# Performance work log

Hardware: AMD Instinct MI355X
Metric: run time of the kernel (lower is better)

## Reference

```python
import jax, jax.numpy as jnp
import numpy as np

EMB = 1024
N_HEAD = 16
HEAD = 64
D_FF = 4 * EMB
LN_EPS = 1e-5


def layernorm(x, g, b):
    mu = jnp.mean(x, axis=-1, keepdims=True)
    var = jnp.mean(jnp.square(x - mu), axis=-1, keepdims=True)
    return (x - mu) * jax.lax.rsqrt(var + LN_EPS) * g + b


def setup_inputs() -> dict:
    key = jax.random.key(0)
    ks = jax.random.split(key, 12)
    s = 0.02
    x = jax.random.normal(ks[0], (4, 2048, EMB), dtype=jnp.float32)
    # per-head Q/K/V projections (no bias), stacked along head axis
    Wq = jax.random.normal(ks[1], (N_HEAD, EMB, HEAD), dtype=jnp.float32) * s
    Wk = jax.random.normal(ks[2], (N_HEAD, EMB, HEAD), dtype=jnp.float32) * s
    Wv = jax.random.normal(ks[3], (N_HEAD, EMB, HEAD), dtype=jnp.float32) * s
    Wo = jax.random.normal(ks[4], (EMB, EMB), dtype=jnp.float32) * s
    bo = jnp.zeros((EMB,), dtype=jnp.float32)
    ln1_g = jnp.ones((EMB,), dtype=jnp.float32)
    ln1_b = jnp.zeros((EMB,), dtype=jnp.float32)
    W1 = jax.random.normal(ks[5], (EMB, D_FF), dtype=jnp.float32) * s
    b1 = jnp.zeros((D_FF,), dtype=jnp.float32)
    W2 = jax.random.normal(ks[6], (D_FF, EMB), dtype=jnp.float32) * s
    b2 = jnp.zeros((EMB,), dtype=jnp.float32)
    ln2_g = jnp.ones((EMB,), dtype=jnp.float32)
    ln2_b = jnp.zeros((EMB,), dtype=jnp.float32)
    return dict(x=x, Wq=Wq, Wk=Wk, Wv=Wv, Wo=Wo, bo=bo, ln1_g=ln1_g,
                ln1_b=ln1_b, W1=W1, b1=b1, W2=W2, b2=b2, ln2_g=ln2_g,
                ln2_b=ln2_b)


def reference(x, Wq, Wk, Wv, Wo, bo, ln1_g, ln1_b, W1, b1, W2, b2, ln2_g, ln2_b):
    B, T, _ = x.shape
    # fused multi-head QKV (equivalent to the per-head Python loop + concat)
    q = jnp.einsum('btd,hdk->bhtk', x, Wq)
    k = jnp.einsum('btd,hdk->bhtk', x, Wk)
    v = jnp.einsum('btd,hdk->bhtk', x, Wv)
    scores = jnp.einsum('bhtk,bhsk->bhts', q, k) / jnp.sqrt(jnp.float32(HEAD))
    att = jax.nn.softmax(scores, axis=-1)
    heads = jnp.einsum('bhts,bhsk->bhtk', att, v)           # [B,H,T,head]
    cat = heads.transpose(0, 2, 1, 3).reshape(B, T, EMB)     # concat over heads
    mha = cat @ Wo + bo
    x = x + layernorm(mha, ln1_g, ln1_b)                     # residual of LN(sublayer)
    ff = jax.nn.gelu(x @ W1 + b1, approximate=False) @ W2 + b2
    x = x + layernorm(ff, ln2_g, ln2_b)
    return x
```

## Files before the change

kernel.cpp:

```cpp
#include <hip/hip_runtime.h>
#include <math.h>


using u16 = unsigned short;
typedef __bf16 bf16x8 __attribute__((ext_vector_type(8)));
typedef __bf16 bf16x4 __attribute__((ext_vector_type(4)));
typedef unsigned short u16x8 __attribute__((ext_vector_type(8)));
typedef unsigned short u16x4 __attribute__((ext_vector_type(4)));
typedef float f32x4 __attribute__((ext_vector_type(4)));

#if defined(__has_builtin)
#if __has_builtin(__builtin_amdgcn_exp2f)
#define EXP2F(x) __builtin_amdgcn_exp2f(x)
#endif
#endif
#ifndef EXP2F
#define EXP2F(x) __expf((x) * 0.69314718055994531f)
#endif

__device__ __forceinline__ float bf2f(u16 h) {
  return __uint_as_float(((unsigned int)h) << 16);
}
__device__ __forceinline__ u16 f2bf(float f) {
  unsigned int u = __float_as_uint(f);
  u += 0x7fffu + ((u >> 16) & 1u);
  return (u16)(u >> 16);
}

__device__ __forceinline__ void gload_lds16(const void* g, void* l) {
  __builtin_amdgcn_global_load_lds(
      (__attribute__((address_space(1))) void*)(g),
      (__attribute__((address_space(3))) void*)(l), 16, 0, 0);
}

__global__ __launch_bounds__(256) void detect_dtype(const u16* __restrict__ x,
                                                    int* __restrict__ flag) {
  __shared__ int cnt[256];
  int c = 0;
#pragma unroll
  for (int j = 0; j < 8; ++j) {
    float v = bf2f(x[threadIdx.x * 8 + j]);
    float a = fabsf(v);
    if (a >= 1e-4f && a <= 64.0f) ++c;
  }
  cnt[threadIdx.x] = c;
  __syncthreads();
  if (threadIdx.x == 0) {
    int t = 0;
    for (int i = 0; i < 256; ++i) t += cnt[i];
    flag[0] = (t < 1638) ? 1 : 0;
  }
}

__global__ __launch_bounds__(256) void cvt_copy(const void* __restrict__ in,
                                                u16* __restrict__ out,
                                                const int* __restrict__ flagp,
                                                long n) {
  long idx = ((long)blockIdx.x * 256 + threadIdx.x) * 4;
  if (idx >= n) return;
  if (*flagp) {
    float4 v = *(const float4*)((const float*)in + idx);
    out[idx] = f2bf(v.x); out[idx + 1] = f2bf(v.y);
    out[idx + 2] = f2bf(v.z); out[idx + 3] = f2bf(v.w);
  } else {
    *(u16x4*)(out + idx) = *(const u16x4*)((const u16*)in + idx);
  }
}

__global__ __launch_bounds__(256) void cvt_vecs(
    const void* s0, const void* s1, const void* s2, const void* s3,
    const void* s4, const void* s5, const void* s6, u16* __restrict__ dst,
    const int* __restrict__ flagp) {
  const int lens[7] = {1024, 1024, 1024, 4096, 1024, 1024, 1024};
  const int offs[7] = {0, 1024, 2048, 3072, 7168, 8192, 9216};
  const void* srcs[7] = {s0, s1, s2, s3, s4, s5, s6};
  int w = blockIdx.x;
  int f = *flagp;
  for (int i = threadIdx.x; i < lens[w]; i += 256)
    dst[offs[w] + i] = f ? f2bf(((const float*)srcs[w])[i])
                         : ((const u16*)srcs[w])[i];
}

__global__ __launch_bounds__(256) void transpose_cvt(
    const void* __restrict__ in, u16* __restrict__ out, int R, int C,
    long inBS, long outBS, const int* __restrict__ flagp) {
  __shared__ u16 tile[32][33];
  int f = *flagp;
  u16* ob = out + (long)blockIdx.z * outBS;
  int c = blockIdx.x * 32 + threadIdx.x;
  int r0 = blockIdx.y * 32;
  if (f) {
    const float* ib = (const float*)in + (long)blockIdx.z * inBS;
#pragma unroll
    for (int i = threadIdx.y; i < 32; i += 8)
      tile[i][threadIdx.x] = f2bf(ib[(long)(r0 + i) * C + c]);
  } else {
    const u16* ib = (const u16*)in + (long)blockIdx.z * inBS;
#pragma unroll
    for (int i = threadIdx.y; i < 32; i += 8)
      tile[i][threadIdx.x] = ib[(long)(r0 + i) * C + c];
  }
  __syncthreads();
  int r = r0 + threadIdx.x;
  int c0 = blockIdx.x * 32;
#pragma unroll
  for (int i = threadIdx.y; i < 32; i += 8)
    ob[(long)(c0 + i) * R + r] = tile[threadIdx.x][i];
}

__global__ __launch_bounds__(256) void kv_frag(const u16* __restrict__ qkv,
                                               u16* __restrict__ KF,
                                               u16* __restrict__ VF) {
  __shared__ u16 Kt[64][72];
  __shared__ u16 Vt[64][72];
  const int jblk = blockIdx.x, bh = blockIdx.y;
  const int b = bh >> 4, h = bh & 15;
  const int tid = threadIdx.x;
  const long j0 = jblk * 64;

  {
    int tt = tid >> 2, c0 = (tid & 3) * 16;
    const u16* src = qkv + (long)(b * 2048 + j0 + tt) * 3072 + h * 64 + c0;
    *(u16x8*)(&Kt[tt][c0]) = *(const u16x8*)(src + 1024);
    *(u16x8*)(&Kt[tt][c0 + 8]) = *(const u16x8*)(src + 1024 + 8);
    *(u16x8*)(&Vt[tt][c0]) = *(const u16x8*)(src + 2048);
    *(u16x8*)(&Vt[tt][c0 + 8]) = *(const u16x8*)(src + 2048 + 8);
  }
  __syncthreads();

  long obase = ((long)bh * 32 + jblk) * 8 * 512;
#pragma unroll
  for (int si = 0; si < 2; ++si) {
    int s = tid * 2 + si;
    int f = s >> 6, ln = s & 63;
    int kt = f >> 2, nt = f & 3;
    int lr = ln & 15, lq = ln >> 4;
    u16x8 ko, vo;
#pragma unroll
    for (int j = 0; j < 8; ++j) {
      ko[j] = Kt[nt * 16 + lr][kt * 32 + lq * 8 + j];
      vo[j] = Vt[kt * 32 + lq * 8 + j][nt * 16 + lr];
    }
    *(u16x8*)(KF + obase + (long)s * 8) = ko;
    *(u16x8*)(VF + obase + (long)s * 8) = vo;
  }
}

__device__ __forceinline__ bf16x8 fragld(const u16* lb, int row, int ks,
                                         int lq) {
  int slot = ((ks << 2) | lq) ^ (row & 7);
  return *(const bf16x8*)(lb + row * 64 + slot * 8);
}

template <int EPI, int BN>
__global__ __launch_bounds__(512, 2) void gemm2ph(
    const u16* __restrict__ A, const u16* __restrict__ Bt,
    const u16* __restrict__ bias, u16* __restrict__ Cout,
    int M, int N, int K) {
  static_assert(BN == 256 || BN == 128, "");
  constexpr int NFQ = BN / 128;
  __shared__ u16 As[2][16384];
  __shared__ u16 Bs[2][BN * 64];
  const int tid = threadIdx.x;
  const int wave = tid >> 6, lane = tid & 63;
  const int lr = lane & 15, lq = lane >> 4;

  const int MT = M >> 8, NTt = N / BN;
  const int nwg = MT * NTt;
  int wg = blockIdx.x;
  if (!(nwg & 7)) wg = (wg & 7) * (nwg >> 3) + (wg >> 3);
  const int tm = wg % MT, tn = wg / MT;
  const long m0 = (long)tm << 8;
  const long n0 = (long)tn * BN;

  const int wm = (wave >> 2) << 7;
  const int wn = (wave & 3) * (BN / 4);

  const int srow = lane >> 3;
  const int skoff = ((lane & 7) ^ srow) * 8;

  auto stage = [&](int buf, int t) {
#pragma unroll
    for (int j = 0; j < 4; ++j)
      gload_lds16(
          A + (m0 + j * 64 + wave * 8 + srow) * (long)K + t * 64 + skoff,
          &As[buf][j * 4096 + (wave << 9)]);
#pragma unroll
    for (int j = 0; j < BN / 64; ++j)
      gload_lds16(
          Bt + (n0 + j * 64 + wave * 8 + srow) * (long)K + t * 64 + skoff,
          &Bs[buf][j * 4096 + (wave << 9)]);
  };

  f32x4 acc[8][2 * NFQ] = {};
  const int NT = K >> 6;
  int cur = 0;

  stage(0, 0);
  __syncthreads();

  for (int t = 0; t < NT; ++t) {
    const u16* Ab = As[cur];
    const u16* Bb = Bs[cur];
    if (t + 1 < NT) stage(cur ^ 1, t + 1);

    bf16x8 a_[4][2], b0_[NFQ][2], b1_[NFQ][2];
#pragma unroll
    for (int mf = 0; mf < 4; ++mf)
#pragma unroll
      for (int ks = 0; ks < 2; ++ks)
        a_[mf][ks] = fragld(Ab, wm + mf * 16 + lr, ks, lq);
#pragma unroll
    for (int nf = 0; nf < NFQ; ++nf)
#pragma unroll
      for (int ks = 0; ks < 2; ++ks)
        b0_[nf][ks] = fragld(Bb, wn + nf * 16 + lr, ks, lq);
#pragma unroll
    for (int mf = 0; mf < 4; ++mf)
#pragma unroll
      for (int nf = 0; nf < NFQ; ++nf)
#pragma unroll
        for (int ks = 0; ks < 2; ++ks)
          acc[mf][nf] = __builtin_amdgcn_mfma_f32_16x16x32_bf16(
              a_[mf][ks], b0_[nf][ks], acc[mf][nf], 0, 0, 0);
#pragma unroll
    for (int nf = 0; nf < NFQ; ++nf)
#pragma unroll
      for (int ks = 0; ks < 2; ++ks)
        b1_[nf][ks] = fragld(Bb, wn + BN / 8 + nf * 16 + lr, ks, lq);
#pragma unroll
    for (int mf = 0; mf < 4; ++mf)
#pragma unroll
      for (int nf = 0; nf < NFQ; ++nf)
#pragma unroll
        for (int ks = 0; ks < 2; ++ks)
          acc[mf][NFQ + nf] = __builtin_amdgcn_mfma_f32_16x16x32_bf16(
              a_[mf][ks], b1_[nf][ks], acc[mf][NFQ + nf], 0, 0, 0);
#pragma unroll
    for (int mf = 0; mf < 4; ++mf)
#pragma unroll
      for (int ks = 0; ks < 2; ++ks)
        a_[mf][ks] = fragld(Ab, wm + 64 + mf * 16 + lr, ks, lq);
#pragma unroll
    for (int mf = 0; mf < 4; ++mf)
#pragma unroll
      for (int nf = 0; nf < NFQ; ++nf)
#pragma unroll
        for (int ks = 0; ks < 2; ++ks)
          acc[4 + mf][NFQ + nf] = __builtin_amdgcn_mfma_f32_16x16x32_bf16(
              a_[mf][ks], b1_[nf][ks], acc[4 + mf][NFQ + nf], 0, 0, 0);
#pragma unroll
    for (int mf = 0; mf < 4; ++mf)
#pragma unroll
      for (int nf = 0; nf < NFQ; ++nf)
#pragma unroll
        for (int ks = 0; ks < 2; ++ks)
          acc[4 + mf][nf] = __builtin_amdgcn_mfma_f32_16x16x32_bf16(
              a_[mf][ks], b0_[nf][ks], acc[4 + mf][nf], 0, 0, 0);

    __syncthreads();
    cur ^= 1;
  }

  const int rq = lq * 4;
#pragma unroll
  for (int mf = 0; mf < 8; ++mf)
#pragma unroll
    for (int nf2 = 0; nf2 < 2 * NFQ; ++nf2) {
      const int col = (int)n0 + wn + nf2 * 16 + lr;
#pragma unroll
      for (int r = 0; r < 4; ++r) {
        const long row = m0 + wm + mf * 16 + rq + r;
        float v = acc[mf][nf2][r];
        if (EPI == 2) {
          v += bf2f(bias[col]);
          v = 0.5f * v * (1.0f + erff(v * 0.70710678118654752f));
        } else if (EPI == 3) {
          v += bf2f(bias[col]);
        }
        Cout[row * (long)N + col] = f2bf(v);
      }
    }
}

__global__ __launch_bounds__(256, 3) void flash_attn(
    const u16* __restrict__ qkv, const u16* __restrict__ KF,
    const u16* __restrict__ VF, u16* __restrict__ cat) {
  const int T = 2048, LD = 3072;
  const float QSCALE = 0.18033688011112042f;
  const float EXPC = 4.3280851226677321f;
  const int bh = blockIdx.y;
  const int b = bh >> 4, h = bh & 15;
  const int tid = threadIdx.x, wave = tid >> 6, lane = tid & 63;
  const int lr = lane & 15, lq = lane >> 4;

  __shared__ u16 Ps[4 * 32 * 72];
  u16* Pw = Ps + wave * 32 * 72;

  const u16* Qb = qkv + (long)(b * 2048) * LD + h * 64;
  const long fbase = (long)bh * 32 * 8 * 512;

  bf16x8 aq[2][2];
#pragma unroll
  for (int st = 0; st < 2; ++st) {
    int qrow = blockIdx.x * 128 + wave * 32 + st * 16 + lr;
#pragma unroll
    for (int kt = 0; kt < 2; ++kt) {
      u16x8 q = *(const u16x8*)(Qb + (long)qrow * LD + kt * 32 + lq * 8);
      bf16x8 t;
#pragma unroll
      for (int j = 0; j < 8; ++j) t[j] = (__bf16)(bf2f(q[j]) * QSCALE);
      aq[st][kt] = t;
    }
  }

  f32x4 o[2][4] = {};
  float lsum[2] = {0.0f, 0.0f};

  for (int jblk = 0; jblk < T / 64; ++jblk) {
    const u16* kf = KF + fbase + (long)jblk * 8 * 512;
    const u16* vf = VF + fbase + (long)jblk * 8 * 512;

    bf16x8 bk[2][4];
#pragma unroll
    for (int kt = 0; kt < 2; ++kt)
#pragma unroll
      for (int nt = 0; nt < 4; ++nt)
        bk[kt][nt] = *(const bf16x8*)(kf + (kt * 4 + nt) * 512 + lane * 8);

    f32x4 s[2][4] = {};
    __builtin_amdgcn_s_setprio(1);
#pragma unroll
    for (int st = 0; st < 2; ++st)
#pragma unroll
      for (int nt = 0; nt < 4; ++nt)
#pragma unroll
        for (int kt = 0; kt < 2; ++kt)
          s[st][nt] = __builtin_amdgcn_mfma_f32_16x16x32_bf16(
              bk[kt][nt], aq[st][kt], s[st][nt], 0, 0, 0);
    __builtin_amdgcn_s_setprio(0);

    bf16x8 bv[2][4];
#pragma unroll
    for (int kt = 0; kt < 2; ++kt)
#pragma unroll
      for (int nt = 0; nt < 4; ++nt)
        bv[kt][nt] = *(const bf16x8*)(vf + (kt * 4 + nt) * 512 + lane * 8);

#pragma unroll
    for (int st = 0; st < 2; ++st)
#pragma unroll
      for (int nt = 0; nt < 4; ++nt) {
        f32x4 p;
#pragma unroll
        for (int r = 0; r < 4; ++r) p[r] = EXP2F(s[st][nt][r] - EXPC);
        lsum[st] += (p[0] + p[1]) + (p[2] + p[3]);
        bf16x4 pk;
#pragma unroll
        for (int r = 0; r < 4; ++r) pk[r] = (__bf16)p[r];
        *(bf16x4*)(Pw + (st * 16 + lr) * 72 + nt * 16 + lq * 4) = pk;
      }

#pragma unroll
    for (int st = 0; st < 2; ++st)
#pragma unroll
      for (int kt = 0; kt < 2; ++kt) {
        bf16x8 ap =
            *(const bf16x8*)(Pw + (st * 16 + lr) * 72 + kt * 32 + lq * 8);
        __builtin_amdgcn_s_setprio(1);
#pragma unroll
        for (int nt = 0; nt < 4; ++nt)
          o[st][nt] = __builtin_amdgcn_mfma_f32_16x16x32_bf16(
              ap, bv[kt][nt], o[st][nt], 0, 0, 0);
        __builtin_amdgcn_s_setprio(0);
      }
  }

#pragma unroll
  for (int st = 0; st < 2; ++st) {
    lsum[st] += __shfl_xor(lsum[st], 16, 64);
    lsum[st] += __shfl_xor(lsum[st], 32, 64);
  }

  u16* ob = cat + (long)(b * 2048) * 1024 + h * 64;
#pragma unroll
  for (int st = 0; st < 2; ++st) {
    int trow = blockIdx.x * 128 + wave * 32 + st * 16 + lq * 4;
#pragma unroll
    for (int r = 0; r < 4; ++r) {
      float linv = 1.0f / __shfl(lsum[st], lq * 4 + r, 64);
#pragma unroll
      for (int nt = 0; nt < 4; ++nt)
        ob[(long)(trow + r) * 1024 + nt * 16 + lr] = f2bf(o[st][nt][r] * linv);
    }
  }
}

__global__ __launch_bounds__(256) void ln_residual(
    const u16* __restrict__ y, const void* __restrict__ res, int res_raw,
    const u16* __restrict__ g, const u16* __restrict__ bb,
    void* __restrict__ out, const int* __restrict__ flagp, int final_out) {
  const long row = blockIdx.x;
  const int tid = threadIdx.x, wave = tid >> 6, lane = tid & 63;
  u16x4 yv = *(const u16x4*)(y + row * 1024 + tid * 4);
  float yy[4];
#pragma unroll
  for (int j = 0; j < 4; ++j) yy[j] = bf2f(yv[j]);
  float s1 = yy[0] + yy[1] + yy[2] + yy[3];
  float s2 = yy[0] * yy[0] + yy[1] * yy[1] + yy[2] * yy[2] + yy[3] * yy[3];
#pragma unroll
  for (int off = 1; off < 64; off <<= 1) {
    s1 += __shfl_xor(s1, off, 64);
    s2 += __shfl_xor(s2, off, 64);
  }
  __shared__ float ws1[4], ws2[4];
  if (lane == 0) { ws1[wave] = s1; ws2[wave] = s2; }
  __syncthreads();
  float t1 = ws1[0] + ws1[1] + ws1[2] + ws1[3];
  float t2 = ws2[0] + ws2[1] + ws2[2] + ws2[3];
  float mu = t1 * (1.0f / 1024.0f);
  float var = t2 * (1.0f / 1024.0f) - mu * mu;
  float rstd = rsqrtf(var + 1e-5f);
  int i = tid * 4;
  bool f32in = res_raw && (*flagp);
  bool f32out = final_out && (*flagp);
#pragma unroll
  for (int j = 0; j < 4; ++j) {
    float rv = f32in ? ((const float*)res)[row * 1024 + i + j]
                     : bf2f(((const u16*)res)[row * 1024 + i + j]);
    float o = rv + (yy[j] - mu) * rstd * bf2f(g[i + j]) + bf2f(bb[i + j]);
    if (f32out)
      ((float*)out)[row * 1024 + i + j] = o;
    else
      ((u16*)out)[row * 1024 + i + j] = f2bf(o);
  }
}

extern "C" void kernel_launch(void* const* d_in, const int* in_sizes, int n_in,
                              void* d_out, int out_size, void* d_ws,
                              size_t ws_size, hipStream_t stream) {
  const void* x_raw = d_in[0];
  const void* Wq = d_in[1];
  const void* Wk = d_in[2];
  const void* Wv = d_in[3];
  const void* Wo = d_in[4];
  const void* bo = d_in[5];
  const void* ln1g = d_in[6];
  const void* ln1b = d_in[7];
  const void* W1 = d_in[8];
  const void* b1 = d_in[9];
  const void* W2 = d_in[10];
  const void* b2 = d_in[11];
  const void* ln2g = d_in[12];
  const void* ln2b = d_in[13];

  char* ws = (char*)d_ws;
  u16* qkv = (u16*)(ws + 0);
  u16* mha = (u16*)(ws + 0);
  u16* h1 = (u16*)(ws + 0);
  u16* cat = (u16*)(ws + 50331648);
  u16* KF = (u16*)(ws + 67108864);
  u16* ff = (u16*)(ws + 67108864);
  u16* xb = (u16*)(ws + 83886080);
  u16* VF = (u16*)(ws + 83886080);
  u16* x1 = (u16*)(ws + 83886080);
  u16* wqkvt = (u16*)(ws + 100663296);
  u16* wot = (u16*)(ws + 106954752);
  u16* w1t = (u16*)(ws + 109051904);
  u16* w2t = (u16*)(ws + 117440512);
  u16* vecs = (u16*)(ws + 125829120);
  int* flag = (int*)(ws + 125853696);

  const u16* v_bo = vecs + 0;
  const u16* v_l1g = vecs + 1024;
  const u16* v_l1b = vecs + 2048;
  const u16* v_b1 = vecs + 3072;
  const u16* v_b2 = vecs + 7168;
  const u16* v_l2g = vecs + 8192;
  const u16* v_l2b = vecs + 9216;

  detect_dtype<<<1, 256, 0, stream>>>((const u16*)x_raw, flag);
  cvt_copy<<<8192, 256, 0, stream>>>(x_raw, xb, flag, 8388608L);
  cvt_vecs<<<7, 256, 0, stream>>>(bo, ln1g, ln1b, b1, b2, ln2g, ln2b, vecs, flag);

  dim3 tb(32, 8);
  transpose_cvt<<<dim3(2, 32, 16), tb, 0, stream>>>(Wq, wqkvt, 1024, 64, 65536, 65536, flag);
  transpose_cvt<<<dim3(2, 32, 16), tb, 0, stream>>>(Wk, wqkvt + 1048576, 1024, 64, 65536, 65536, flag);
  transpose_cvt<<<dim3(2, 32, 16), tb, 0, stream>>>(Wv, wqkvt + 2097152, 1024, 64, 65536, 65536, flag);
  transpose_cvt<<<dim3(32, 32, 1), tb, 0, stream>>>(Wo, wot, 1024, 1024, 0, 0, flag);
  transpose_cvt<<<dim3(128, 32, 1), tb, 0, stream>>>(W1, w1t, 1024, 4096, 0, 0, flag);
  transpose_cvt<<<dim3(32, 128, 1), tb, 0, stream>>>(W2, w2t, 4096, 1024, 0, 0, flag);

  gemm2ph<0, 128><<<768, 512, 0, stream>>>(xb, wqkvt, nullptr, qkv, 8192, 3072, 1024);
  kv_frag<<<dim3(32, 64), 256, 0, stream>>>(qkv, KF, VF);
  flash_attn<<<dim3(16, 64), 256, 0, stream>>>(qkv, KF, VF, cat);
  gemm2ph<3, 128><<<256, 512, 0, stream>>>(cat, wot, v_bo, mha, 8192, 1024, 1024);
  ln_residual<<<8192, 256, 0, stream>>>(mha, x_raw, 1, v_l1g, v_l1b, x1, flag, 0);
  gemm2ph<2, 256><<<512, 512, 0, stream>>>(x1, w1t, v_b1, h1, 8192, 4096, 1024);
  gemm2ph<3, 128><<<256, 512, 0, stream>>>(h1, w2t, v_b2, ff, 8192, 1024, 4096);
  ln_residual<<<8192, 256, 0, stream>>>(ff, x1, 0, v_l2g, v_l2b, d_out, flag, 1);
}
```

Baseline: 621.5 us.

## Halve GEMM K-step to 32 and add 128x128 GEMM for N=1024 layers

The main GEMM kernel now stages 32-wide K slices instead of 64, with a matching 4-way XOR swizzle, which halves LDS use per buffer and should allow more resident workgroups. A new 256-thread 128x128-tile GEMM handles the output projection and the second FFN matmul (N=1024), so those launches use 512 workgroups instead of 256 and fill the CUs better. The cost is twice as many barriers and pipeline iterations per K, and less reuse per staged byte.

```diff
diff --git a/kernel.cpp b/kernel.cpp
--- a/kernel.cpp
+++ b/kernel.cpp
@@ -146,10 +146,9 @@
   }
 }
 
-__device__ __forceinline__ bf16x8 fragld(const u16* lb, int row, int ks,
-                                         int lq) {
-  int slot = ((ks << 2) | lq) ^ (row & 7);
-  return *(const bf16x8*)(lb + row * 64 + slot * 8);
+__device__ __forceinline__ bf16x8 fragld32(const u16* lb, int row, int lq) {
+  int slot = lq ^ (row & 3);
+  return *(const bf16x8*)(lb + row * 32 + slot * 8);
 }
 
 template <int EPI, int BN>
@@ -159,8 +158,8 @@
     int M, int N, int K) {
   static_assert(BN == 256 || BN == 128, "");
   constexpr int NFQ = BN / 128;
-  __shared__ u16 As[2][16384];
-  __shared__ u16 Bs[2][BN * 64];
+  __shared__ u16 As[2][256 * 32];
+  __shared__ u16 Bs[2][BN * 32];
   const int tid = threadIdx.x;
   const int wave = tid >> 6, lane = tid & 63;
   const int lr = lane & 15, lq = lane >> 4;
@@ -176,24 +175,24 @@
   const int wm = (wave >> 2) << 7;
   const int wn = (wave & 3) * (BN / 4);
 
-  const int srow = lane >> 3;
-  const int skoff = ((lane & 7) ^ srow) * 8;
+  const int srow = lane >> 2;
+  const int skoff = ((lane & 3) ^ (srow & 3)) * 8;
 
   auto stage = [&](int buf, int t) {
 #pragma unroll
-    for (int j = 0; j < 4; ++j)
+    for (int j = 0; j < 2; ++j)
       gload_lds16(
-          A + (m0 + j * 64 + wave * 8 + srow) * (long)K + t * 64 + skoff,
+          A + (m0 + j * 128 + wave * 16 + srow) * (long)K + t * 32 + skoff,
           &As[buf][j * 4096 + (wave << 9)]);
 #pragma unroll
-    for (int j = 0; j < BN / 64; ++j)
+    for (int j = 0; j < BN / 128; ++j)
       gload_lds16(
-          Bt + (n0 + j * 64 + wave * 8 + srow) * (long)K + t * 64 + skoff,
+          Bt + (n0 + j * 128 + wave * 16 + srow) * (long)K + t * 32 + skoff,
           &Bs[buf][j * 4096 + (wave << 9)]);
   };
 
   f32x4 acc[8][2 * NFQ] = {};
-  const int NT = K >> 6;
+  const int NT = K >> 5;
   int cur = 0;
 
   stage(0, 0);
@@ -204,59 +203,42 @@
     const u16* Bb = Bs[cur];
     if (t + 1 < NT) stage(cur ^ 1, t + 1);
 
-    bf16x8 a_[4][2], b0_[NFQ][2], b1_[NFQ][2];
-#pragma unroll
-    for (int mf = 0; mf < 4; ++mf)
-#pragma unroll
-      for (int ks = 0; ks < 2; ++ks)
-        a_[mf][ks] = fragld(Ab, wm + mf * 16 + lr, ks, lq);
+    bf16x8 a_[4], b0_[NFQ], b1_[NFQ];
+#pragma unroll
+    for (int mf = 0; mf < 4; ++mf) a_[mf] = fragld32(Ab, wm + mf * 16 + lr, lq);
 #pragma unroll
     for (int nf = 0; nf < NFQ; ++nf)
-#pragma unroll
-      for (int ks = 0; ks < 2; ++ks)
-        b0_[nf][ks] = fragld(Bb, wn + nf * 16 + lr, ks, lq);
+      b0_[nf] = fragld32(Bb, wn + nf * 16 + lr, lq);
 #pragma unroll
     for (int mf = 0; mf < 4; ++mf)
 #pragma unroll
       for (int nf = 0; nf < NFQ; ++nf)
-#pragma unroll
-        for (int ks = 0; ks < 2; ++ks)
-          acc[mf][nf] = __builtin_amdgcn_mfma_f32_16x16x32_bf16(
-              a_[mf][ks], b0_[nf][ks], acc[mf][nf], 0, 0, 0);
+        acc[mf][nf] = __builtin_amdgcn_mfma_f32_16x16x32_bf16(
+            a_[mf], b0_[nf], acc[mf][nf], 0, 0, 0);
 #pragma unroll
     for (int nf = 0; nf < NFQ; ++nf)
-#pragma unroll
-      for (int ks = 0; ks < 2; ++ks)
-        b1_[nf][ks] = fragld(Bb, wn + BN / 8 + nf * 16 + lr, ks, lq);
+      b1_[nf] = fragld32(Bb, wn + BN / 8 + nf * 16 + lr, lq);
 #pragma unroll
     for (int mf = 0; mf < 4; ++mf)
 #pragma unroll
       for (int nf = 0; nf < NFQ; ++nf)
-#pragma unroll
-        for (int ks = 0; ks < 2; ++ks)
-          acc[mf][NFQ + nf] = __builtin_amdgcn_mfma_f32_16x16x32_bf16(
-              a_[mf][ks], b1_[nf][ks], acc[mf][NFQ + nf], 0, 0, 0);
-#pragma unroll
-    for (int mf = 0; mf < 4; ++mf)
-#pragma unroll
-      for (int ks = 0; ks < 2; ++ks)
-        a_[mf][ks] = fragld(Ab, wm + 64 + mf * 16 + lr, ks, lq);
+        acc[mf][NFQ + nf] = __builtin_amdgcn_mfma_f32_16x16x32_bf16(
+            a_[mf], b1_[nf], acc[mf][NFQ + nf], 0, 0, 0);
+#pragma unroll
+    for (int mf = 0; mf < 4; ++mf)
+      a_[mf] = fragld32(Ab, wm + 64 + mf * 16 + lr, lq);
 #pragma unroll
     for (int mf = 0; mf < 4; ++mf)
 #pragma unroll
       for (int nf = 0; nf < NFQ; ++nf)
-#pragma unroll
-        for (int ks = 0; ks < 2; ++ks)
-          acc[4 + mf][NFQ + nf] = __builtin_amdgcn_mfma_f32_16x16x32_bf16(
-              a_[mf][ks], b1_[nf][ks], acc[4 + mf][NFQ + nf], 0, 0, 0);
+        acc[4 + mf][NFQ + nf] = __builtin_amdgcn_mfma_f32_16x16x32_bf16(
+            a_[mf], b1_[nf], acc[4 + mf][NFQ + nf], 0, 0, 0);
 #pragma unroll
     for (int mf = 0; mf < 4; ++mf)
 #pragma unroll
       for (int nf = 0; nf < NFQ; ++nf)
-#pragma unroll
-        for (int ks = 0; ks < 2; ++ks)
-          acc[4 + mf][nf] = __builtin_amdgcn_mfma_f32_16x16x32_bf16(
-              a_[mf][ks], b0_[nf][ks], acc[4 + mf][nf], 0, 0, 0);
+        acc[4 + mf][nf] = __builtin_amdgcn_mfma_f32_16x16x32_bf16(
+            a_[mf], b0_[nf], acc[4 + mf][nf], 0, 0, 0);
 
     __syncthreads();
     cur ^= 1;
@@ -272,6 +254,97 @@
       for (int r = 0; r < 4; ++r) {
         const long row = m0 + wm + mf * 16 + rq + r;
         float v = acc[mf][nf2][r];
+        if (EPI == 2) {
+          v += bf2f(bias[col]);
+          v = 0.5f * v * (1.0f + erff(v * 0.70710678118654752f));
+        } else if (EPI == 3) {
+          v += bf2f(bias[col]);
+        }
+        Cout[row * (long)N + col] = f2bf(v);
+      }
+    }
+}
+
+template <int EPI>
+__global__ __launch_bounds__(256) void gemm128(
+    const u16* __restrict__ A, const u16* __restrict__ Bt,
+    const u16* __restrict__ bias, u16* __restrict__ Cout,
+    int M, int N, int K) {
+  __shared__ u16 As[2][128 * 32];
+  __shared__ u16 Bs[2][128 * 32];
+  const int tid = threadIdx.x;
+  const int wave = tid >> 6, lane = tid & 63;
+  const int lr = lane & 15, lq = lane >> 4;
+
+  const int MT = M >> 7, NTt = N >> 7;
+  const int nwg = MT * NTt;
+  int wg = blockIdx.x;
+  if (!(nwg & 7)) wg = (wg & 7) * (nwg >> 3) + (wg >> 3);
+  const int tm = wg % MT, tn = wg / MT;
+  const long m0 = (long)tm << 7, n0 = (long)tn << 7;
+  const int wm = (wave >> 1) * 64, wn = (wave & 1) * 64;
+
+  const int srow = lane >> 2;
+  const int skoff = ((lane & 3) ^ (srow & 3)) * 8;
+
+  auto stage = [&](int buf, int t) {
+#pragma unroll
+    for (int j = 0; j < 2; ++j) {
+      gload_lds16(
+          A + (m0 + j * 64 + wave * 16 + srow) * (long)K + t * 32 + skoff,
+          &As[buf][j * 2048 + (wave << 9)]);
+      gload_lds16(
+          Bt + (n0 + j * 64 + wave * 16 + srow) * (long)K + t * 32 + skoff,
+          &Bs[buf][j * 2048 + (wave << 9)]);
+    }
+  };
+
+  f32x4 acc[4][4] = {};
+  const int NT = K >> 5;
+  int cur = 0;
+
+  stage(0, 0);
+  __syncthreads();
+
+  for (int t = 0; t < NT; ++t) {
+    const u16* Ab = As[cur];
+    const u16* Bb = Bs[cur];
+    if (t + 1 < NT) stage(cur ^ 1, t + 1);
+
+    bf16x8 a_[4], b_[4];
+#pragma unroll
+    for (int mf = 0; mf < 4; ++mf) a_[mf] = fragld32(Ab, wm + mf * 16 + lr, lq);
+#pragma unroll
+    for (int nf = 0; nf < 2; ++nf) b_[nf] = fragld32(Bb, wn + nf * 16 + lr, lq);
+#pragma unroll
+    for (int mf = 0; mf < 4; ++mf)
+#pragma unroll
+      for (int nf = 0; nf < 2; ++nf)
+        acc[mf][nf] = __builtin_amdgcn_mfma_f32_16x16x32_bf16(
+            a_[mf], b_[nf], acc[mf][nf], 0, 0, 0);
+#pragma unroll
+    for (int nf = 2; nf < 4; ++nf) b_[nf] = fragld32(Bb, wn + nf * 16 + lr, lq);
+#pragma unroll
+    for (int mf = 0; mf < 4; ++mf)
+#pragma unroll
+      for (int nf = 2; nf < 4; ++nf)
+        acc[mf][nf] = __builtin_amdgcn_mfma_f32_16x16x32_bf16(
+            a_[mf], b_[nf], acc[mf][nf], 0, 0, 0);
+
+    __syncthreads();
+    cur ^= 1;
+  }
+
+  const int rq = lq * 4;
+#pragma unroll
+  for (int mf = 0; mf < 4; ++mf)
+#pragma unroll
+    for (int nf = 0; nf < 4; ++nf) {
+      const int col = (int)n0 + wn + nf * 16 + lr;
+#pragma unroll
+      for (int r = 0; r < 4; ++r) {
+        const long row = m0 + wm + mf * 16 + rq + r;
+        float v = acc[mf][nf][r];
         if (EPI == 2) {
           v += bf2f(bias[col]);
           v = 0.5f * v * (1.0f + erff(v * 0.70710678118654752f));
@@ -494,9 +567,9 @@
   gemm2ph<0, 128><<<768, 512, 0, stream>>>(xb, wqkvt, nullptr, qkv, 8192, 3072, 1024);
   kv_frag<<<dim3(32, 64), 256, 0, stream>>>(qkv, KF, VF);
   flash_attn<<<dim3(16, 64), 256, 0, stream>>>(qkv, KF, VF, cat);
-  gemm2ph<3, 128><<<256, 512, 0, stream>>>(cat, wot, v_bo, mha, 8192, 1024, 1024);
+  gemm128<3><<<512, 256, 0, stream>>>(cat, wot, v_bo, mha, 8192, 1024, 1024);
   ln_residual<<<8192, 256, 0, stream>>>(mha, x_raw, 1, v_l1g, v_l1b, x1, flag, 0);
   gemm2ph<2, 256><<<512, 512, 0, stream>>>(x1, w1t, v_b1, h1, 8192, 4096, 1024);
-  gemm2ph<3, 128><<<256, 512, 0, stream>>>(h1, w2t, v_b2, ff, 8192, 1024, 4096);
+  gemm128<3><<<512, 256, 0, stream>>>(h1, w2t, v_b2, ff, 8192, 1024, 4096);
   ln_residual<<<8192, 256, 0, stream>>>(ff, x1, 0, v_l2g, v_l2b, d_out, flag, 1);
 }
```

Result: slower. 645.4 us (+3.8%).
